# Kernel tuning notes

Hardware: AMD Instinct MI355X
Metric: run time of the kernel (lower is better)

The kernel has to match this reference:

```python
import jax, jax.numpy as jnp
import numpy as np
from jax import lax

B, T, D, LSTM, N_MELS, SPK, NOISE = 256, 600, 256, 512, 80, 256, 64
MAX_R = 10
FC1 = 256
FC2 = D // 2  # 128
FILTERS, KSIZE = 32, 31


def _lin(k, out_d, in_d):
    return jax.random.normal(k, (out_d, in_d), jnp.float32) * 0.02


def setup_inputs() -> dict:
    key = jax.random.key(0)
    ks = list(jax.random.split(key, 40))
    nk = iter(ks)
    inp = {
        "encoder_seq": jax.random.normal(next(nk), (B, T, D), jnp.float32),
        "encoder_seq_proj": jax.random.normal(next(nk), (B, T, D), jnp.float32),
        "prenet_in": jax.random.normal(next(nk), (B, N_MELS), jnp.float32),
        "attn_hidden": jax.random.normal(next(nk), (B, D), jnp.float32),
        "rnn1_hidden": jax.random.normal(next(nk), (B, LSTM), jnp.float32),
        "rnn2_hidden": jax.random.normal(next(nk), (B, LSTM), jnp.float32),
        "rnn1_cell": jax.random.normal(next(nk), (B, LSTM), jnp.float32),
        "rnn2_cell": jax.random.normal(next(nk), (B, LSTM), jnp.float32),
        "context_vec": jax.random.normal(next(nk), (B, D), jnp.float32),
        "speaker_embedding": jax.random.normal(next(nk), (B, SPK), jnp.float32),
        "noise_embedding": jax.random.normal(next(nk), (B, NOISE), jnp.float32),
        "attn_cumulative": jax.random.uniform(next(nk), (B, T), jnp.float32),
        "attn_prev": jax.random.uniform(next(nk), (B, T), jnp.float32),
        "phone_len": jax.random.randint(next(nk), (B,), 1, T + 1),
        # PreNet
        "fc1_w": _lin(next(nk), FC1, N_MELS + NOISE), "fc1_b": jnp.zeros((FC1,), jnp.float32),
        "fc2_w": _lin(next(nk), FC2, FC1), "fc2_b": jnp.zeros((FC2,), jnp.float32),
        # LSA
        "conv_w": jax.random.normal(next(nk), (FILTERS, 2, KSIZE), jnp.float32) * 0.1,
        "L_w": _lin(next(nk), D, FILTERS), "L_b": jnp.zeros((D,), jnp.float32),
        "W_w": _lin(next(nk), D, D), "W_b": jnp.zeros((D,), jnp.float32),
        "v_w": _lin(next(nk), 1, D),
        # attn GRU: input = D + D//2 + SPK
        "gru_wih": _lin(next(nk), 3 * D, D + FC2 + SPK), "gru_whh": _lin(next(nk), 3 * D, D),
        "gru_bih": jnp.zeros((3 * D,), jnp.float32), "gru_bhh": jnp.zeros((3 * D,), jnp.float32),
        # rnn_input Linear: 2*D + SPK + NOISE -> LSTM
        "rnn_in_w": _lin(next(nk), LSTM, 2 * D + SPK + NOISE), "rnn_in_b": jnp.zeros((LSTM,), jnp.float32),
        # two LSTMCells
        "l1_wih": _lin(next(nk), 4 * LSTM, LSTM), "l1_whh": _lin(next(nk), 4 * LSTM, LSTM),
        "l1_bih": jnp.zeros((4 * LSTM,), jnp.float32), "l1_bhh": jnp.zeros((4 * LSTM,), jnp.float32),
        "l2_wih": _lin(next(nk), 4 * LSTM, LSTM), "l2_whh": _lin(next(nk), 4 * LSTM, LSTM),
        "l2_bih": jnp.zeros((4 * LSTM,), jnp.float32), "l2_bhh": jnp.zeros((4 * LSTM,), jnp.float32),
        # mel projection (no bias)
        "mel_w": _lin(next(nk), N_MELS * MAX_R, LSTM),
        "r": 2,
    }
    return inp


def _gru(x, h, wih, whh, bih, bhh):
    gi = x @ wih.T + bih
    gh = h @ whh.T + bhh
    i_r, i_z, i_n = jnp.split(gi, 3, axis=-1)
    h_r, h_z, h_n = jnp.split(gh, 3, axis=-1)
    r = jax.nn.sigmoid(i_r + h_r)
    z = jax.nn.sigmoid(i_z + h_z)
    n = jnp.tanh(i_n + r * h_n)
    return (1.0 - z) * n + z * h


def _lstm(x, h, c, wih, whh, bih, bhh):
    g = x @ wih.T + bih + h @ whh.T + bhh
    i, f, gg, o = jnp.split(g, 4, axis=-1)
    c_new = jax.nn.sigmoid(f) * c + jax.nn.sigmoid(i) * jnp.tanh(gg)
    h_new = jax.nn.sigmoid(o) * jnp.tanh(c_new)
    return h_new, c_new


def reference(encoder_seq, encoder_seq_proj, prenet_in, attn_hidden, rnn1_hidden,
              rnn2_hidden, rnn1_cell, rnn2_cell, context_vec, speaker_embedding,
              noise_embedding, attn_cumulative, attn_prev, phone_len,
              fc1_w, fc1_b, fc2_w, fc2_b, conv_w, L_w, L_b, W_w, W_b, v_w,
              gru_wih, gru_whh, gru_bih, gru_bhh, rnn_in_w, rnn_in_b,
              l1_wih, l1_whh, l1_bih, l1_bhh, l2_wih, l2_whh, l2_bih, l2_bhh,
              mel_w, r):
    # PreNet (eval-mode: dropout omitted for a deterministic reference)
    p = jnp.concatenate([prenet_in, noise_embedding], axis=-1)
    p = jax.nn.relu(p @ fc1_w.T + fc1_b)
    prenet_out = jax.nn.relu(p @ fc2_w.T + fc2_b)

    # attention GRU
    attn_rnn_in = jnp.concatenate([context_vec, prenet_out, speaker_embedding], axis=-1)
    attn_hidden = _gru(attn_rnn_in, attn_hidden, gru_wih, gru_whh, gru_bih, gru_bhh)

    # location-sensitive attention (t > 0 step; state passed explicitly)
    pq = (attn_hidden @ W_w.T + W_b)[:, None, :]                     # [B,1,D]
    location = jnp.stack([attn_cumulative, attn_prev], axis=1)       # [B,2,T]
    loc = lax.conv_general_dilated(location, conv_w, (1,), [((KSIZE - 1) // 2,) * 2],
                                   dimension_numbers=("NCH", "OIH", "NCH"))  # [B,F,T]
    pl = jnp.einsum("bft,df->btd", loc, L_w) + L_b                   # [B,T,D]
    u = jnp.einsum("btd,od->bt", jnp.tanh(pq + encoder_seq_proj + pl), v_w)
    mask = jnp.arange(T)[None, :] < phone_len[:, None]
    u = jnp.where(mask, u, -1e9)
    scores_bt = jax.nn.softmax(u, axis=1)                            # [B,T]
    scores = scores_bt[:, None, :]                                   # [B,1,T]

    context_vec = jnp.einsum("bt,btd->bd", scores_bt, encoder_seq)   # [B,D]

    x = jnp.concatenate([context_vec, attn_hidden, speaker_embedding, noise_embedding], axis=1)
    x = x @ rnn_in_w.T + rnn_in_b

    rnn1_hidden, rnn1_cell = _lstm(x, rnn1_hidden, rnn1_cell, l1_wih, l1_whh, l1_bih, l1_bhh)
    x = x + rnn1_hidden
    rnn2_hidden, rnn2_cell = _lstm(x, rnn2_hidden, rnn2_cell, l2_wih, l2_whh, l2_bih, l2_bhh)
    x = x + rnn2_hidden

    mels = (x @ mel_w.T).reshape(B, N_MELS, MAX_R)[:, :, :r]
    return (mels, scores, attn_hidden, rnn1_hidden, rnn2_hidden, rnn1_cell, rnn2_cell, context_vec)
```

## Files before the change

kernel.cpp:

```cpp
#include <hip/hip_runtime.h>
#include <hip/hip_bf16.h>
#include <cstdint>

#define B_ 256
#define T_ 600
#define D_ 256

typedef __attribute__((ext_vector_type(8))) short bf16x8;
typedef __attribute__((ext_vector_type(4))) float f32x4;

__device__ __forceinline__ float fast_sigmoid(float x) {
    return __fdividef(1.0f, 1.0f + __expf(-x));
}
__device__ __forceinline__ float fast_tanh(float x) {
    return 1.0f - __fdividef(2.0f, __expf(2.0f * x) + 1.0f);
}
__device__ __forceinline__ ushort f2bf(float f) {
    unsigned u = __float_as_uint(f);
    u += 0x7FFF + ((u >> 16) & 1);
    return (ushort)(u >> 16);
}
__device__ __forceinline__ float bf2f(ushort u) {
    return __uint_as_float((unsigned)u << 16);
}

__global__ __launch_bounds__(256) void prenet_kernel(
    const float* __restrict__ pre_in, const float* __restrict__ noise,
    const float* __restrict__ w1, const float* __restrict__ b1,
    const float* __restrict__ w2, const float* __restrict__ b2,
    const float* __restrict__ ctx_in, const float* __restrict__ spk,
    const float* __restrict__ L_w, ushort* __restrict__ Lw16,
    ushort* __restrict__ Xgru16, ushort* __restrict__ Xrnn16)
{
    __shared__ float xin[144];
    __shared__ float p1[256];
    int b = blockIdx.x, t = threadIdx.x;
    if (b == 0) {
        for (int o = t; o < 8192; o += 256) {
            int dt = o >> 9;
            int ln = (o >> 3) & 63;
            int j  = o & 7;
            int in_idx = (dt * 16 + (ln & 15)) * 32 + (ln >> 4) * 8 + j;
            Lw16[o] = f2bf(L_w[in_idx]);
        }
    }
    float s = spk[b * 256 + t];
    Xgru16[b * 640 + t] = f2bf(ctx_in[b * 256 + t]);
    Xgru16[b * 640 + 384 + t] = f2bf(s);
    Xrnn16[b * 832 + 512 + t] = f2bf(s);
    if (t < 64) Xrnn16[b * 832 + 768 + t] = f2bf(noise[b * 64 + t]);
    if (t < 80) xin[t] = pre_in[b * 80 + t];
    else if (t < 144) xin[t] = noise[b * 64 + (t - 80)];
    __syncthreads();
    float acc = b1[t];
    const float4* w = (const float4*)(w1 + t * 144);
    const float4* xi = (const float4*)xin;
#pragma unroll 9
    for (int k = 0; k < 36; ++k) {
        float4 wv = w[k]; float4 xv = xi[k];
        acc += wv.x * xv.x + wv.y * xv.y + wv.z * xv.z + wv.w * xv.w;
    }
    p1[t] = fmaxf(acc, 0.f);
    __syncthreads();
    if (t < 128) {
        float a2 = b2[t];
        const float4* w2v = (const float4*)(w2 + t * 256);
        const float4* pv = (const float4*)p1;
#pragma unroll 8
        for (int k = 0; k < 64; ++k) {
            float4 wv = w2v[k]; float4 xv = pv[k];
            a2 += wv.x * xv.x + wv.y * xv.y + wv.z * xv.z + wv.w * xv.w;
        }
        Xgru16[b * 640 + 256 + t] = f2bf(fmaxf(a2, 0.f));
    }
}

__global__ __launch_bounds__(256) void convert_all(
    const float* __restrict__ w1ih, const float* __restrict__ w1hh,
    const float* __restrict__ w2ih, const float* __restrict__ w2hh,
    const float* __restrict__ gwih, const float* __restrict__ gwhh,
    const float* __restrict__ Ww, const float* __restrict__ riw,
    const float* __restrict__ ahin, const float* __restrict__ h1in,
    ushort* __restrict__ wcat1, ushort* __restrict__ wcat2,
    ushort* __restrict__ gwih16, ushort* __restrict__ gwhh16,
    ushort* __restrict__ Ww16, ushort* __restrict__ riw16,
    ushort* __restrict__ ahin16, ushort* __restrict__ xh1)
{
    int bid = blockIdx.x, t = threadIdx.x;
    if (bid < 4096) {
        int n = bid & 2047;
        int layer = bid >> 11;
        const float* wih = layer ? w2ih : w1ih;
        const float* whh = layer ? w2hh : w1hh;
        ushort* dst = layer ? wcat2 : wcat1;
        const float* src = (t < 128) ? (wih + (size_t)n * 512 + t * 4)
                                     : (whh + (size_t)n * 512 + (t - 128) * 4);
        float4 v = *(const float4*)src;
        ushort4 o;
        o.x = f2bf(v.x); o.y = f2bf(v.y); o.z = f2bf(v.z); o.w = f2bf(v.w);
        *(ushort4*)&dst[(size_t)n * 1024 + t * 4] = o;
        return;
    }
    bid -= 4096;
    if (bid >= 1216) {
        bid -= 1216;
        size_t i = (size_t)bid * 1024 + t * 4;
        float4 v = *(const float4*)&h1in[i];
        int b = (int)(i >> 9), k = (int)(i & 511);
        ushort4 o;
        o.x = f2bf(v.x); o.y = f2bf(v.y); o.z = f2bf(v.z); o.w = f2bf(v.w);
        *(ushort4*)&xh1[(size_t)b * 1024 + 512 + k] = o;
        return;
    }
    const float* src; ushort* dst;
    if (bid < 480)       { src = gwih; dst = gwih16; }
    else if (bid < 672)  { bid -= 480;  src = gwhh; dst = gwhh16; }
    else if (bid < 736)  { bid -= 672;  src = Ww;   dst = Ww16; }
    else if (bid < 1152) { bid -= 736;  src = riw;  dst = riw16; }
    else                 { bid -= 1152; src = ahin; dst = ahin16; }
    size_t i = (size_t)bid * 1024 + t * 4;
    float4 v = *(const float4*)&src[i];
    ushort4 o;
    o.x = f2bf(v.x); o.y = f2bf(v.y); o.z = f2bf(v.z); o.w = f2bf(v.w);
    *(ushort4*)&dst[i] = o;
}

__global__ __launch_bounds__(256) void mfma_gemmN(
    const ushort* __restrict__ A16, int K,
    const ushort* __restrict__ B16, const float* __restrict__ bias,
    float* __restrict__ C, int N, ushort* __restrict__ xcast)
{
    int tid = threadIdx.x;
    int lane = tid & 63, wv = tid >> 6;
    int m0 = blockIdx.x * 32;
    int n0 = blockIdx.y * 64;
    int wm = wv >> 1, wn = wv & 1;
    int cl = lane & 15, ko = (lane >> 4) * 8;

    const ushort* ap  = A16 + (size_t)(m0 + wm * 16 + cl) * K + ko;
    const ushort* bp0 = B16 + (size_t)(n0 + wn * 32 + cl) * K + ko;
    const ushort* bp1 = bp0 + (size_t)16 * K;

    f32x4 acc0 = {0.f, 0.f, 0.f, 0.f};
    f32x4 acc1 = {0.f, 0.f, 0.f, 0.f};
    int nks = K >> 5;
#pragma unroll 2
    for (int ks = 0; ks < nks; ++ks) {
        bf16x8 a  = *(const bf16x8*)ap;
        bf16x8 b0 = *(const bf16x8*)bp0;
        bf16x8 b1 = *(const bf16x8*)bp1;
        ap += 32; bp0 += 32; bp1 += 32;
        acc0 = __builtin_amdgcn_mfma_f32_16x16x32_bf16(a, b0, acc0, 0, 0, 0);
        acc1 = __builtin_amdgcn_mfma_f32_16x16x32_bf16(a, b1, acc1, 0, 0, 0);
    }
    int orow = m0 + wm * 16 + (lane >> 4) * 4;
    int ocol = n0 + wn * 32 + cl;
    float bb0 = bias ? bias[ocol] : 0.f;
    float bb1 = bias ? bias[ocol + 16] : 0.f;
#pragma unroll
    for (int r2 = 0; r2 < 4; ++r2) {
        float v0 = acc0[r2] + bb0;
        float v1 = acc1[r2] + bb1;
        C[(size_t)(orow + r2) * N + ocol]      = v0;
        C[(size_t)(orow + r2) * N + ocol + 16] = v1;
        if (xcast) {
            xcast[(size_t)(orow + r2) * 1024 + ocol]      = f2bf(v0);
            xcast[(size_t)(orow + r2) * 1024 + ocol + 16] = f2bf(v1);
        }
    }
}

__global__ __launch_bounds__(256) void mfma_gemm(
    const ushort* __restrict__ A16, const ushort* __restrict__ B16,
    float* __restrict__ G0, float* __restrict__ G1)
{
    int tid = threadIdx.x;
    int lane = tid & 63, wv = tid >> 6;
    int m0 = blockIdx.x * 32;
    int n0 = blockIdx.y * 64;
    int kbase = blockIdx.z * 512;
    float* Gout = blockIdx.z ? G1 : G0;
    int wm = wv >> 1, wn = wv & 1;
    int cl = lane & 15, ko = (lane >> 4) * 8;

    const ushort* ap  = A16 + (size_t)(m0 + wm * 16 + cl) * 1024 + kbase + ko;
    const ushort* bp0 = B16 + (size_t)(n0 + wn * 32 + cl) * 1024 + kbase + ko;
    const ushort* bp1 = bp0 + (size_t)16 * 1024;

    f32x4 acc0 = {0.f, 0.f, 0.f, 0.f};
    f32x4 acc1 = {0.f, 0.f, 0.f, 0.f};
#pragma unroll
    for (int ks = 0; ks < 16; ++ks) {
        bf16x8 a  = *(const bf16x8*)(ap  + ks * 32);
        bf16x8 b0 = *(const bf16x8*)(bp0 + ks * 32);
        bf16x8 b1 = *(const bf16x8*)(bp1 + ks * 32);
        acc0 = __builtin_amdgcn_mfma_f32_16x16x32_bf16(a, b0, acc0, 0, 0, 0);
        acc1 = __builtin_amdgcn_mfma_f32_16x16x32_bf16(a, b1, acc1, 0, 0, 0);
    }
    int orow = m0 + wm * 16 + (lane >> 4) * 4;
    int ocol = n0 + wn * 32 + cl;
#pragma unroll
    for (int r2 = 0; r2 < 4; ++r2) {
        Gout[(size_t)(orow + r2) * 2048 + ocol]      = acc0[r2];
        Gout[(size_t)(orow + r2) * 2048 + ocol + 16] = acc1[r2];
    }
}

__global__ __launch_bounds__(256) void gru_combine(
    const float* __restrict__ Cgi, const float* __restrict__ Cgh,
    const float* __restrict__ h_in, float* __restrict__ ah_out,
    ushort* __restrict__ ah16, ushort* __restrict__ Xrnn16)
{
    int b = blockIdx.x, j = threadIdx.x;
    float gir = Cgi[b * 768 + j], giz = Cgi[b * 768 + 256 + j], gin = Cgi[b * 768 + 512 + j];
    float ghr = Cgh[b * 768 + j], ghz = Cgh[b * 768 + 256 + j], ghn = Cgh[b * 768 + 512 + j];
    float rr = fast_sigmoid(gir + ghr);
    float zz = fast_sigmoid(giz + ghz);
    float nn = fast_tanh(gin + rr * ghn);
    float h = (1.f - zz) * nn + zz * h_in[b * 256 + j];
    ah_out[b * 256 + j] = h;
    ah16[b * 256 + j] = f2bf(h);
    Xrnn16[b * 832 + 256 + j] = f2bf(h);
}

#define PLP 264
__global__ __launch_bounds__(1024) void attn_u_kernel(
    const float* __restrict__ esp, const float* __restrict__ pq,
    const float* __restrict__ cum, const float* __restrict__ prv,
    const float* __restrict__ conv_w, const ushort* __restrict__ Lw16,
    const float* __restrict__ L_b, const float* __restrict__ v_w,
    float* __restrict__ u)
{
    __shared__ float cumL[96], prvL[96];
    __shared__ float cwL[1984];
    __shared__ ushort lwS[8192];
    __shared__ ushort locs[64][40];
    __shared__ ushort plS[64 * PLP];
    __shared__ float pq2s[256], vvs[256];
    int b = blockIdx.y;
    int t0 = blockIdx.x * 64;
    int tid = threadIdx.x;
    int lane = tid & 63, w = tid >> 6;
    int tt = w & 3, dtg = w >> 2;
    int cl = lane & 15, gr = lane >> 4;

    for (int i = tid; i < 94; i += 1024) {
        int tg = t0 + i - 15;
        bool ok = (tg >= 0) && (tg < T_);
        cumL[i] = ok ? cum[b * T_ + tg] : 0.f;
        prvL[i] = ok ? prv[b * T_ + tg] : 0.f;
    }
    for (int i = tid; i < 1984; i += 1024) cwL[i] = conv_w[i];
    {
        const float4* src = (const float4*)Lw16;
        float4* dst = (float4*)lwS;
        dst[tid] = src[tid];
    }
    if (tid < 256) {
        pq2s[tid] = pq[b * 256 + tid] + L_b[tid];
        vvs[tid] = v_w[tid];
    }
    __syncthreads();

    {
        int f = tid & 31, ts = tid >> 5;
        const float* c0 = &cwL[f * 62];
        float a0 = 0.f, a1 = 0.f;
#pragma unroll
        for (int k = 0; k < 31; ++k) {
            float wcv = c0[k], wpv = c0[31 + k];
            a0 = fmaf(cumL[ts + k], wcv, fmaf(prvL[ts + k], wpv, a0));
            a1 = fmaf(cumL[ts + 32 + k], wcv, fmaf(prvL[ts + 32 + k], wpv, a1));
        }
        locs[ts][f] = f2bf(a0);
        locs[ts + 32][f] = f2bf(a1);
    }
    __syncthreads();

    {
        bf16x8 locf = *(const bf16x8*)&locs[tt * 16 + cl][gr * 8];
#pragma unroll
        for (int j = 0; j < 4; ++j) {
            int dt = dtg * 4 + j;
            bf16x8 af = *(const bf16x8*)&lwS[(dt * 64 + lane) * 8];
            f32x4 acc = {0.f, 0.f, 0.f, 0.f};
            acc = __builtin_amdgcn_mfma_f32_16x16x32_bf16(af, locf, acc, 0, 0, 0);
            ushort4 pk;
            pk.x = f2bf(acc[0]); pk.y = f2bf(acc[1]);
            pk.z = f2bf(acc[2]); pk.w = f2bf(acc[3]);
            *(ushort4*)&plS[(tt * 16 + cl) * PLP + dt * 16 + gr * 4] = pk;
        }
    }
    __syncthreads();

    float4 pq4 = *(const float4*)&pq2s[lane * 4];
    float4 vv4 = *(const float4*)&vvs[lane * 4];
#pragma unroll
    for (int rr = 0; rr < 4; ++rr) {
        int row = w + rr * 16;
        int tg = t0 + row;
        int tc = (tg < T_) ? tg : (T_ - 1);
        float4 e4 = *((const float4*)(esp + ((size_t)b * T_ + tc) * 256) + lane);
        ushort4 pl4 = *(const ushort4*)&plS[row * PLP + lane * 4];
        float s = 0.f;
        s = fmaf(fast_tanh(e4.x + pq4.x + bf2f(pl4.x)), vv4.x, s);
        s = fmaf(fast_tanh(e4.y + pq4.y + bf2f(pl4.y)), vv4.y, s);
        s = fmaf(fast_tanh(e4.z + pq4.z + bf2f(pl4.z)), vv4.z, s);
        s = fmaf(fast_tanh(e4.w + pq4.w + bf2f(pl4.w)), vv4.w, s);
#pragma unroll
        for (int off = 32; off > 0; off >>= 1) s += __shfl_xor(s, off, 64);
        if (lane == 0 && tg < T_) u[b * T_ + tg] = s;
    }
}

__global__ __launch_bounds__(1024) void softmax_ctx_kernel(
    const float* __restrict__ u, const int* __restrict__ plen,
    const float* __restrict__ enc,
    float* __restrict__ scores, float* __restrict__ ctx_out,
    ushort* __restrict__ Xrnn16)
{
    __shared__ float sc[T_];
    __shared__ float red[16];
    __shared__ float part[16][256];
    int b = blockIdx.x, tid = threadIdx.x;
    int lane = tid & 63, wid = tid >> 6;
    int pl = plen[b];
    float mv = -1e30f;
    if (tid < T_) {
        float uv = u[b * T_ + tid];
        mv = (tid < pl) ? uv : -1e9f;
        sc[tid] = mv;
    }
    float m = mv;
#pragma unroll
    for (int off = 32; off > 0; off >>= 1) m = fmaxf(m, __shfl_xor(m, off, 64));
    if (lane == 0) red[wid] = m;
    __syncthreads();
    m = red[0];
#pragma unroll
    for (int i = 1; i < 16; ++i) m = fmaxf(m, red[i]);
    float ev = 0.f;
    if (tid < T_) ev = __expf(sc[tid] - m);
    float s = ev;
    __syncthreads();
#pragma unroll
    for (int off = 32; off > 0; off >>= 1) s += __shfl_xor(s, off, 64);
    if (lane == 0) red[wid] = s;
    __syncthreads();
    float tot = 0.f;
#pragma unroll
    for (int i = 0; i < 16; ++i) tot += red[i];
    float inv = __fdividef(1.0f, tot);
    if (tid < T_) {
        float scv = ev * inv;
        scores[b * T_ + tid] = scv;
        sc[tid] = scv;
    }
    __syncthreads();
    float a0 = 0.f, a1 = 0.f, a2 = 0.f, a3 = 0.f;
    const float4* ep = (const float4*)(enc + ((size_t)b * T_ + wid) * 256) + lane;
    for (int t = wid; t < T_; t += 16) {
        float sv = sc[t];
        float4 ev4 = *ep;
        a0 = fmaf(sv, ev4.x, a0);
        a1 = fmaf(sv, ev4.y, a1);
        a2 = fmaf(sv, ev4.z, a2);
        a3 = fmaf(sv, ev4.w, a3);
        ep += 16 * 64;
    }
    part[wid][lane * 4 + 0] = a0;
    part[wid][lane * 4 + 1] = a1;
    part[wid][lane * 4 + 2] = a2;
    part[wid][lane * 4 + 3] = a3;
    __syncthreads();
    if (tid < 256) {
        float c = 0.f;
#pragma unroll
        for (int q = 0; q < 16; ++q) c += part[q][tid];
        ctx_out[b * 256 + tid] = c;
        Xrnn16[b * 832 + tid] = f2bf(c);
    }
}

__global__ __launch_bounds__(512) void lstm_combine2(
    const float* __restrict__ G0, const float* __restrict__ G1,
    const float* __restrict__ bih, const float* __restrict__ bhh,
    const float* __restrict__ c_in, const float* __restrict__ x_in,
    float* __restrict__ h_out, float* __restrict__ c_out,
    float* __restrict__ x_next,
    const float* __restrict__ h_next_in, ushort* __restrict__ xh_next)
{
    int b = blockIdx.x, j = threadIdx.x;
    size_t base = (size_t)b * 2048;
    float gi = G0[base + j] + G1[base + j] + bih[j] + bhh[j];
    float gf = G0[base + 512 + j] + G1[base + 512 + j] + bih[512 + j] + bhh[512 + j];
    float gg = G0[base + 1024 + j] + G1[base + 1024 + j] + bih[1024 + j] + bhh[1024 + j];
    float go = G0[base + 1536 + j] + G1[base + 1536 + j] + bih[1536 + j] + bhh[1536 + j];
    float c = fast_sigmoid(gf) * c_in[b * 512 + j] + fast_sigmoid(gi) * fast_tanh(gg);
    float h = fast_sigmoid(go) * fast_tanh(c);
    float xn = x_in[b * 512 + j] + h;
    h_out[b * 512 + j] = h;
    c_out[b * 512 + j] = c;
    x_next[b * 512 + j] = xn;
    if (xh_next) {
        xh_next[(size_t)b * 1024 + j] = f2bf(xn);
        xh_next[(size_t)b * 1024 + 512 + j] = f2bf(h_next_in[b * 512 + j]);
    }
}

__global__ __launch_bounds__(256) void mel_kernel(
    const float* __restrict__ x2, const float* __restrict__ mel_w,
    int r, float* __restrict__ mels)
{
    __shared__ float xl[512];
    int b = blockIdx.x, tid = threadIdx.x;
    xl[tid] = x2[b * 512 + tid];
    xl[256 + tid] = x2[b * 512 + 256 + tid];
    __syncthreads();
    for (int idx = tid; idx < 80 * r; idx += 256) {
        int mrow = (idx / r) * 10 + (idx % r);
        const float4* w = (const float4*)(mel_w + (size_t)mrow * 512);
        const float4* xv = (const float4*)xl;
        float acc = 0.f;
#pragma unroll 16
        for (int k = 0; k < 128; ++k) {
            float4 a = w[k], c = xv[k];
            acc += a.x * c.x + a.y * c.y + a.z * c.z + a.w * c.w;
        }
        mels[(size_t)b * 80 * r + idx] = acc;
    }
}

extern "C" void kernel_launch(void* const* d_in, const int* in_sizes, int n_in,
                              void* d_out, int out_size, void* d_ws, size_t ws_size,
                              hipStream_t stream)
{
    const float* enc    = (const float*)d_in[0];
    const float* esp    = (const float*)d_in[1];
    const float* pre_in = (const float*)d_in[2];
    const float* ah_in  = (const float*)d_in[3];
    const float* h1_in  = (const float*)d_in[4];
    const float* h2_in  = (const float*)d_in[5];
    const float* c1_in  = (const float*)d_in[6];
    const float* c2_in  = (const float*)d_in[7];
    const float* ctx_in = (const float*)d_in[8];
    const float* spk    = (const float*)d_in[9];
    const float* noise  = (const float*)d_in[10];
    const float* cum    = (const float*)d_in[11];
    const float* prv    = (const float*)d_in[12];
    const int*   plen   = (const int*)d_in[13];
    const float* fc1_w  = (const float*)d_in[14];
    const float* fc1_b  = (const float*)d_in[15];
    const float* fc2_w  = (const float*)d_in[16];
    const float* fc2_b  = (const float*)d_in[17];
    const float* conv_w = (const float*)d_in[18];
    const float* L_w    = (const float*)d_in[19];
    const float* L_b    = (const float*)d_in[20];
    const float* W_w    = (const float*)d_in[21];
    const float* W_b    = (const float*)d_in[22];
    const float* v_w    = (const float*)d_in[23];
    const float* g_wih  = (const float*)d_in[24];
    const float* g_whh  = (const float*)d_in[25];
    const float* g_bih  = (const float*)d_in[26];
    const float* g_bhh  = (const float*)d_in[27];
    const float* ri_w   = (const float*)d_in[28];
    const float* ri_b   = (const float*)d_in[29];
    const float* l1_wih = (const float*)d_in[30];
    const float* l1_whh = (const float*)d_in[31];
    const float* l1_bih = (const float*)d_in[32];
    const float* l1_bhh = (const float*)d_in[33];
    const float* l2_wih = (const float*)d_in[34];
    const float* l2_whh = (const float*)d_in[35];
    const float* l2_bih = (const float*)d_in[36];
    const float* l2_bhh = (const float*)d_in[37];
    const float* mel_w  = (const float*)d_in[38];

    int r = (out_size - 808960) / 20480;
    if (r < 1) r = 1;
    if (r > 10) r = 10;

    float* out    = (float*)d_out;
    float* mels   = out;
    float* scores = out + (size_t)20480 * r;
    float* ah_out = scores + 153600;
    float* h1_out = ah_out + 65536;
    float* h2_out = h1_out + 131072;
    float* c1_out = h2_out + 131072;
    float* c2_out = c1_out + 131072;
    float* ctx_out = c2_out + 131072;

    float* ws   = (float*)d_ws;
    float* Cgi  = ws;
    float* Cgh  = Cgi + 196608;
    float* pq   = Cgh + 196608;
    float* uu   = pq + 65536;
    float* x0   = uu + 153600;
    float* x1   = x0 + 131072;
    float* x2   = x1 + 131072;
    float* G0   = x2 + 131072;
    float* G1   = G0 + 524288;
    ushort* Lw16   = (ushort*)(G1 + 524288);
    ushort* Xgru16 = Lw16 + 8192;
    ushort* Xrnn16 = Xgru16 + 163840;
    ushort* ah16   = Xrnn16 + 212992;
    ushort* ahin16 = ah16 + 65536;
    ushort* wcat1  = ahin16 + 65536;
    ushort* wcat2  = wcat1 + 2097152;
    ushort* gwih16 = wcat2 + 2097152;
    ushort* gwhh16 = gwih16 + 491520;
    ushort* Ww16   = gwhh16 + 196608;
    ushort* riw16  = Ww16 + 65536;
    ushort* xh1    = riw16 + 425984;
    ushort* xh2    = xh1 + 262144;

    prenet_kernel<<<256, 256, 0, stream>>>(pre_in, noise, fc1_w, fc1_b, fc2_w, fc2_b,
                                           ctx_in, spk, L_w, Lw16, Xgru16, Xrnn16);
    convert_all<<<5440, 256, 0, stream>>>(l1_wih, l1_whh, l2_wih, l2_whh,
                                          g_wih, g_whh, W_w, ri_w, ah_in, h1_in,
                                          wcat1, wcat2, gwih16, gwhh16,
                                          Ww16, riw16, ahin16, xh1);
    mfma_gemmN<<<dim3(8, 12), 256, 0, stream>>>(Xgru16, 640, gwih16, g_bih, Cgi, 768, nullptr);
    mfma_gemmN<<<dim3(8, 12), 256, 0, stream>>>(ahin16, 256, gwhh16, g_bhh, Cgh, 768, nullptr);
    gru_combine<<<256, 256, 0, stream>>>(Cgi, Cgh, ah_in, ah_out, ah16, Xrnn16);
    mfma_gemmN<<<dim3(8, 4), 256, 0, stream>>>(ah16, 256, Ww16, W_b, pq, 256, nullptr);
    attn_u_kernel<<<dim3(10, 256), 1024, 0, stream>>>(esp, pq, cum, prv, conv_w, Lw16, L_b, v_w, uu);
    softmax_ctx_kernel<<<256, 1024, 0, stream>>>(uu, plen, enc, scores, ctx_out, Xrnn16);
    mfma_gemmN<<<dim3(8, 8), 256, 0, stream>>>(Xrnn16, 832, riw16, ri_b, x0, 512, xh1);
    mfma_gemm<<<dim3(8, 32, 2), 256, 0, stream>>>(xh1, wcat1, G0, G1);
    lstm_combine2<<<256, 512, 0, stream>>>(G0, G1, l1_bih, l1_bhh, c1_in, x0,
                                           h1_out, c1_out, x1, h2_in, xh2);
    mfma_gemm<<<dim3(8, 32, 2), 256, 0, stream>>>(xh2, wcat2, G0, G1);
    lstm_combine2<<<256, 512, 0, stream>>>(G0, G1, l2_bih, l2_bhh, c2_in, x1,
                                           h2_out, c2_out, x2, nullptr, nullptr);
    mel_kernel<<<256, 256, 0, stream>>>(x2, mel_w, r, mels);
}
```

Measured before the change: 207.1 us.

## Process all time chunks per batch in one attention block with register conv weights

Result: slower. 221.3 us (+6.8%).

```diff
diff --git a/kernel.cpp b/kernel.cpp
--- a/kernel.cpp
+++ b/kernel.cpp
@@ -231,26 +231,31 @@
     const float* __restrict__ L_b, const float* __restrict__ v_w,
     float* __restrict__ u)
 {
-    __shared__ float cumL[96], prvL[96];
-    __shared__ float cwL[1984];
+    __shared__ float cumF[672], prvF[672];
     __shared__ ushort lwS[8192];
     __shared__ ushort locs[64][40];
     __shared__ ushort plS[64 * PLP];
     __shared__ float pq2s[256], vvs[256];
-    int b = blockIdx.y;
-    int t0 = blockIdx.x * 64;
+    int b = blockIdx.x;
     int tid = threadIdx.x;
     int lane = tid & 63, w = tid >> 6;
     int tt = w & 3, dtg = w >> 2;
     int cl = lane & 15, gr = lane >> 4;
-
-    for (int i = tid; i < 94; i += 1024) {
-        int tg = t0 + i - 15;
+    int f = tid & 31, ts5 = tid >> 5;
+
+    float wc[31], wp[31];
+#pragma unroll
+    for (int k = 0; k < 31; ++k) {
+        wc[k] = conv_w[f * 62 + k];
+        wp[k] = conv_w[f * 62 + 31 + k];
+    }
+
+    for (int i = tid; i < 672; i += 1024) {
+        int tg = i - 15;
         bool ok = (tg >= 0) && (tg < T_);
-        cumL[i] = ok ? cum[b * T_ + tg] : 0.f;
-        prvL[i] = ok ? prv[b * T_ + tg] : 0.f;
-    }
-    for (int i = tid; i < 1984; i += 1024) cwL[i] = conv_w[i];
+        cumF[i] = ok ? cum[b * T_ + tg] : 0.f;
+        prvF[i] = ok ? prv[b * T_ + tg] : 0.f;
+    }
     {
         const float4* src = (const float4*)Lw16;
         float4* dst = (float4*)lwS;
@@ -262,54 +267,54 @@
     }
     __syncthreads();
 
-    {
-        int f = tid & 31, ts = tid >> 5;
-        const float* c0 = &cwL[f * 62];
-        float a0 = 0.f, a1 = 0.f;
-#pragma unroll
-        for (int k = 0; k < 31; ++k) {
-            float wcv = c0[k], wpv = c0[31 + k];
-            a0 = fmaf(cumL[ts + k], wcv, fmaf(prvL[ts + k], wpv, a0));
-            a1 = fmaf(cumL[ts + 32 + k], wcv, fmaf(prvL[ts + 32 + k], wpv, a1));
-        }
-        locs[ts][f] = f2bf(a0);
-        locs[ts + 32][f] = f2bf(a1);
-    }
-    __syncthreads();
-
-    {
-        bf16x8 locf = *(const bf16x8*)&locs[tt * 16 + cl][gr * 8];
-#pragma unroll
-        for (int j = 0; j < 4; ++j) {
-            int dt = dtg * 4 + j;
-            bf16x8 af = *(const bf16x8*)&lwS[(dt * 64 + lane) * 8];
-            f32x4 acc = {0.f, 0.f, 0.f, 0.f};
-            acc = __builtin_amdgcn_mfma_f32_16x16x32_bf16(af, locf, acc, 0, 0, 0);
-            ushort4 pk;
-            pk.x = f2bf(acc[0]); pk.y = f2bf(acc[1]);
-            pk.z = f2bf(acc[2]); pk.w = f2bf(acc[3]);
-            *(ushort4*)&plS[(tt * 16 + cl) * PLP + dt * 16 + gr * 4] = pk;
-        }
-    }
-    __syncthreads();
-
     float4 pq4 = *(const float4*)&pq2s[lane * 4];
     float4 vv4 = *(const float4*)&vvs[lane * 4];
-#pragma unroll
-    for (int rr = 0; rr < 4; ++rr) {
-        int row = w + rr * 16;
-        int tg = t0 + row;
-        int tc = (tg < T_) ? tg : (T_ - 1);
-        float4 e4 = *((const float4*)(esp + ((size_t)b * T_ + tc) * 256) + lane);
-        ushort4 pl4 = *(const ushort4*)&plS[row * PLP + lane * 4];
-        float s = 0.f;
-        s = fmaf(fast_tanh(e4.x + pq4.x + bf2f(pl4.x)), vv4.x, s);
-        s = fmaf(fast_tanh(e4.y + pq4.y + bf2f(pl4.y)), vv4.y, s);
-        s = fmaf(fast_tanh(e4.z + pq4.z + bf2f(pl4.z)), vv4.z, s);
-        s = fmaf(fast_tanh(e4.w + pq4.w + bf2f(pl4.w)), vv4.w, s);
-#pragma unroll
-        for (int off = 32; off > 0; off >>= 1) s += __shfl_xor(s, off, 64);
-        if (lane == 0 && tg < T_) u[b * T_ + tg] = s;
+
+    for (int ch = 0; ch < 10; ++ch) {
+        int t0 = ch * 64;
+        {
+            float a0 = 0.f, a1 = 0.f;
+#pragma unroll
+            for (int k = 0; k < 31; ++k) {
+                a0 = fmaf(cumF[t0 + ts5 + k], wc[k], fmaf(prvF[t0 + ts5 + k], wp[k], a0));
+                a1 = fmaf(cumF[t0 + ts5 + 32 + k], wc[k], fmaf(prvF[t0 + ts5 + 32 + k], wp[k], a1));
+            }
+            locs[ts5][f] = f2bf(a0);
+            locs[ts5 + 32][f] = f2bf(a1);
+        }
+        __syncthreads();
+        {
+            bf16x8 locf = *(const bf16x8*)&locs[tt * 16 + cl][gr * 8];
+#pragma unroll
+            for (int j = 0; j < 4; ++j) {
+                int dt = dtg * 4 + j;
+                bf16x8 af = *(const bf16x8*)&lwS[(dt * 64 + lane) * 8];
+                f32x4 acc = {0.f, 0.f, 0.f, 0.f};
+                acc = __builtin_amdgcn_mfma_f32_16x16x32_bf16(af, locf, acc, 0, 0, 0);
+                ushort4 pk;
+                pk.x = f2bf(acc[0]); pk.y = f2bf(acc[1]);
+                pk.z = f2bf(acc[2]); pk.w = f2bf(acc[3]);
+                *(ushort4*)&plS[(tt * 16 + cl) * PLP + dt * 16 + gr * 4] = pk;
+            }
+        }
+        __syncthreads();
+#pragma unroll
+        for (int rr = 0; rr < 4; ++rr) {
+            int row = w + rr * 16;
+            int tg = t0 + row;
+            int tc = (tg < T_) ? tg : (T_ - 1);
+            float4 e4 = *((const float4*)(esp + ((size_t)b * T_ + tc) * 256) + lane);
+            ushort4 pl4 = *(const ushort4*)&plS[row * PLP + lane * 4];
+            float s = 0.f;
+            s = fmaf(fast_tanh(e4.x + pq4.x + bf2f(pl4.x)), vv4.x, s);
+            s = fmaf(fast_tanh(e4.y + pq4.y + bf2f(pl4.y)), vv4.y, s);
+            s = fmaf(fast_tanh(e4.z + pq4.z + bf2f(pl4.z)), vv4.z, s);
+            s = fmaf(fast_tanh(e4.w + pq4.w + bf2f(pl4.w)), vv4.w, s);
+#pragma unroll
+            for (int off = 32; off > 0; off >>= 1) s += __shfl_xor(s, off, 64);
+            if (lane == 0 && tg < T_) u[b * T_ + tg] = s;
+        }
+        __syncthreads();
     }
 }
 
@@ -523,7 +528,7 @@
     mfma_gemmN<<<dim3(8, 12), 256, 0, stream>>>(ahin16, 256, gwhh16, g_bhh, Cgh, 768, nullptr);
     gru_combine<<<256, 256, 0, stream>>>(Cgi, Cgh, ah_in, ah_out, ah16, Xrnn16);
     mfma_gemmN<<<dim3(8, 4), 256, 0, stream>>>(ah16, 256, Ww16, W_b, pq, 256, nullptr);
-    attn_u_kernel<<<dim3(10, 256), 1024, 0, stream>>>(esp, pq, cum, prv, conv_w, Lw16, L_b, v_w, uu);
+    attn_u_kernel<<<256, 1024, 0, stream>>>(esp, pq, cum, prv, conv_w, Lw16, L_b, v_w, uu);
     softmax_ctx_kernel<<<256, 1024, 0, stream>>>(uu, plen, enc, scores, ctx_out, Xrnn16);
     mfma_gemmN<<<dim3(8, 8), 256, 0, stream>>>(Xrnn16, 832, riw16, ri_b, x0, 512, xh1);
     mfma_gemm<<<dim3(8, 32, 2), 256, 0, stream>>>(xh1, wcat1, G0, G1);
```
